# Kernel optimization log

Measured on AMD Instinct MI355X. Metric: run time of the kernel, lower is better.

Reference implementation:

```python
import jax, jax.numpy as jnp
import numpy as np
import math

N_HEADS = 12
ROPE_DIM = 64
BASE = 10000.0


def _rope_tables(seq_len, dim):
    inv_freq = 1.0 / (BASE ** (jnp.arange(0, dim, 2, dtype=jnp.float32) / dim))
    t = jnp.arange(seq_len, dtype=jnp.float32)
    freqs = jnp.outer(t, inv_freq)                      # [S, dim/2]
    emb = jnp.concatenate([freqs, freqs], axis=-1)      # [S, dim]
    # broadcast shape [1, S, 1, dim]
    return jnp.cos(emb)[None, :, None, :], jnp.sin(emb)[None, :, None, :]


def _rotate_half(x):
    x1, x2 = jnp.split(x, 2, axis=-1)
    return jnp.concatenate([-x2, x1], axis=-1)


def setup_inputs() -> dict:
    key = jax.random.key(0)
    ks = jax.random.split(key, 9)
    B, S, E = 2, 2048, 768
    s = 1.0 / math.sqrt(E)
    return {
        "x": jax.random.normal(ks[0], (B, S, E), jnp.float32),
        "Wq": jax.random.normal(ks[1], (E, E), jnp.float32) * s,
        "bq": jax.random.normal(ks[2], (E,), jnp.float32) * 0.02,
        "Wk": jax.random.normal(ks[3], (E, E), jnp.float32) * s,
        "bk": jax.random.normal(ks[4], (E,), jnp.float32) * 0.02,
        "Wv": jax.random.normal(ks[5], (E, E), jnp.float32) * s,
        "bv": jax.random.normal(ks[6], (E,), jnp.float32) * 0.02,
        "Wp": jax.random.normal(ks[7], (E, E), jnp.float32) * s,
        "bp": jax.random.normal(ks[8], (E,), jnp.float32) * 0.02,
    }


def reference(x, Wq, bq, Wk, bk, Wv, bv, Wp, bp):
    B, S, E = x.shape
    H = N_HEADS
    D = E // H

    q = (x @ Wq + bq).reshape(B, S, H, D)
    k = (x @ Wk + bk).reshape(B, S, H, D)
    v = (x @ Wv + bv).reshape(B, S, H, D)

    # rotary on first ROPE_DIM dims (here ROPE_DIM == D, so full rotary)
    cos, sin = _rope_tables(S, ROPE_DIM)
    q_rot, q_pass = q[..., :ROPE_DIM], q[..., ROPE_DIM:]
    k_rot, k_pass = k[..., :ROPE_DIM], k[..., ROPE_DIM:]
    q_rot = q_rot * cos + _rotate_half(q_rot) * sin
    k_rot = k_rot * cos + _rotate_half(k_rot) * sin
    q = jnp.concatenate([q_rot, q_pass], axis=-1)
    k = jnp.concatenate([k_rot, k_pass], axis=-1)

    # scores [B, M, N, H]; mask before scaling (as in the torch code; -inf unchanged)
    att = jnp.einsum("bmhd,bnhd->bmnh", q, k)
    causal = jnp.tril(jnp.ones((S, S), dtype=bool))[None, :, :, None]
    att = jnp.where(causal, att, -jnp.inf)
    att = jax.nn.softmax(att / math.sqrt(D), axis=2)
    out = jnp.einsum("bmnh,bnhd->bmhd", att, v)

    return out.reshape(B, S, E) @ Wp + bp
```

## Files before the change

kernel.cpp:

```cpp
#include <hip/hip_runtime.h>
#include <stdint.h>

#define S_LEN 2048
#define EMB   768
#define NH    12
#define DH    64
#define M_TOT 4096
#define WELEM 589824
#define QELEM 3145728

typedef float  floatx4 __attribute__((ext_vector_type(4)));
typedef __bf16 bf16x8  __attribute__((ext_vector_type(8)));
typedef __bf16 bf16x4  __attribute__((ext_vector_type(4)));
typedef unsigned short ushortx4 __attribute__((ext_vector_type(4)));

__device__ __forceinline__ unsigned short f2bf(float f) {
    union { float f; unsigned u; } v; v.f = f;
    unsigned u = v.u;
    unsigned r = (u + 0x7FFFu + ((u >> 16) & 1u)) >> 16;
    return (unsigned short)r;
}

__device__ __forceinline__ void gl_lds16(const void* g, void* l) {
    __builtin_amdgcn_global_load_lds(
        (__attribute__((address_space(1))) const void*)g,
        (__attribute__((address_space(3))) void*)l, 16, 0, 0);
}

__global__ void cvt_all_kernel(const float* __restrict__ x, unsigned short* __restrict__ xb,
                               const float* __restrict__ W0, const float* __restrict__ W1,
                               const float* __restrict__ W2, const float* __restrict__ W3,
                               unsigned short* __restrict__ WT_all) {
    __shared__ float t[64][65];
    const int blk = blockIdx.x;
    if (blk < 3072) {
        int i = (blk * 256 + threadIdx.x) * 4;
        float4 v = *(const float4*)(x + i);
        ushortx4 r = { f2bf(v.x), f2bf(v.y), f2bf(v.z), f2bf(v.w) };
        *(ushortx4*)(xb + i) = r;
        return;
    }
    const int tc = blk - 3072;
    const int z = tc / 144, rr0 = tc % 144;
    const float* W = (z == 0) ? W0 : (z == 1 ? W1 : (z == 2 ? W2 : W3));
    unsigned short* O = WT_all + (size_t)z * WELEM;
    const int k0 = (rr0 % 12) * 64, n0 = (rr0 / 12) * 64;
    const int c = threadIdx.x & 63, r4 = threadIdx.x >> 6;
#pragma unroll
    for (int rr = 0; rr < 64; rr += 4) {
        int r = rr + r4;
        t[r][c] = W[(size_t)(k0 + r) * EMB + n0 + c];
    }
    __syncthreads();
#pragma unroll
    for (int rr = 0; rr < 64; rr += 4) {
        int nn = rr + r4;
        O[(size_t)(n0 + nn) * EMB + k0 + c] = f2bf(t[c][nn]);
    }
}

static __device__ __forceinline__ void gemm_core_128x128(
    const unsigned short* __restrict__ A, const unsigned short* __restrict__ BT,
    int m0, int n0, int K, int tid, floatx4 (&acc)[4][4],
    unsigned short* Als, unsigned short* Bls)
{
    const int lane = tid & 63;
    const int c0 = lane & 15, quad = lane >> 4;
    const int wave = tid >> 6;
    const int wm = (wave >> 1) * 64, wn = (wave & 1) * 64;

    for (int k0 = 0; k0 < K; k0 += 64) {
        __syncthreads();
#pragma unroll
        for (int it = 0; it < 4; ++it) {
            int ch = it * 256 + tid;
            int row = ch >> 3, sc = ch & 7;
            int cc = sc ^ (row & 7);
            gl_lds16(A  + (size_t)(m0 + row) * K + k0 + cc * 8, Als + ch * 8);
            gl_lds16(BT + (size_t)(n0 + row) * K + k0 + cc * 8, Bls + ch * 8);
        }
        __syncthreads();
        bf16x8 af[4][2], bfv[4][2];
#pragma unroll
        for (int ii = 0; ii < 4; ++ii) {
            int row = wm + 16 * ii + c0;
#pragma unroll
            for (int h = 0; h < 2; ++h)
                af[ii][h] = *(const bf16x8*)(Als + row * 64 + (((4 * h + quad) ^ (row & 7)) * 8));
        }
#pragma unroll
        for (int jj = 0; jj < 4; ++jj) {
            int row = wn + 16 * jj + c0;
#pragma unroll
            for (int h = 0; h < 2; ++h)
                bfv[jj][h] = *(const bf16x8*)(Bls + row * 64 + (((4 * h + quad) ^ (row & 7)) * 8));
        }
#pragma unroll
        for (int ii = 0; ii < 4; ++ii)
#pragma unroll
            for (int jj = 0; jj < 4; ++jj) {
                acc[ii][jj] = __builtin_amdgcn_mfma_f32_16x16x32_bf16(af[ii][0], bfv[jj][0], acc[ii][jj], 0, 0, 0);
                acc[ii][jj] = __builtin_amdgcn_mfma_f32_16x16x32_bf16(af[ii][1], bfv[jj][1], acc[ii][jj], 0, 0, 0);
            }
    }
}

__global__ __launch_bounds__(256, 2) void qkv_kernel(
    const unsigned short* __restrict__ xb, const unsigned short* __restrict__ WT_all,
    const float* __restrict__ bq, const float* __restrict__ bk, const float* __restrict__ bv,
    unsigned short* __restrict__ qkv_out)
{
    __shared__ __align__(16) unsigned short Als[128 * 64];
    __shared__ __align__(16) unsigned short Bls[128 * 64];
    const int z = blockIdx.z;
    const float* bias = (z == 0) ? bq : (z == 1 ? bk : bv);
    __bf16* Cout = (__bf16*)(qkv_out + (size_t)z * QELEM);
    const int m0 = blockIdx.x * 128, n0 = blockIdx.y * 128;
    const int tid = threadIdx.x, lane = tid & 63, c0 = lane & 15, quad = lane >> 4, wave = tid >> 6;
    const int wm = (wave >> 1) * 64, wn = (wave & 1) * 64;

    floatx4 acc[4][4] = {};
    gemm_core_128x128(xb, WT_all + (size_t)z * WELEM, m0, n0, EMB, tid, acc, Als, Bls);

#pragma unroll
    for (int ii = 0; ii < 4; ++ii) {
#pragma unroll
        for (int r = 0; r < 4; ++r) {
            int m = m0 + wm + 16 * ii + quad * 4 + r;
            int b = m >> 11, s = m & (S_LEN - 1);
            float vals[4];
#pragma unroll
            for (int jj = 0; jj < 4; ++jj) vals[jj] = acc[ii][jj][r] + bias[n0 + wn + 16 * jj + c0];
            if (z < 2) {
#pragma unroll
                for (int jj = 0; jj < 2; ++jj) {
                    int d = 16 * jj + c0;
                    float f = exp2f((float)d * -0.41524101186092034f);
                    float th = (float)s * f;
                    float sn, cs; sincosf(th, &sn, &cs);
                    float lo = vals[jj], hi = vals[jj + 2];
                    vals[jj]     = lo * cs - hi * sn;
                    vals[jj + 2] = hi * cs + lo * sn;
                }
            }
            if (z == 0) {
#pragma unroll
                for (int jj = 0; jj < 4; ++jj) vals[jj] *= 0.18033688011112042f;
            }
#pragma unroll
            for (int jj = 0; jj < 4; ++jj) {
                int n = n0 + wn + 16 * jj + c0;
                int h = n >> 6, d = n & 63;
                if (z < 2)
                    Cout[((size_t)(b * NH + h) * S_LEN + s) * DH + d] = (__bf16)vals[jj];
                else
                    Cout[((size_t)(b * NH + h) * DH + d) * S_LEN + s] = (__bf16)vals[jj];
            }
        }
    }
}

__global__ __launch_bounds__(256, 2) void flash_kernel(
    const unsigned short* __restrict__ Qg, const unsigned short* __restrict__ Kg,
    const unsigned short* __restrict__ Vt, unsigned short* __restrict__ Og)
{
    __shared__ __align__(16) unsigned short Kls[2][64 * 64];
    __shared__ __align__(16) unsigned short Vls[2][64 * 64];
    __shared__ __align__(16) unsigned short Pls[4][16 * 72];

    const int i = blockIdx.x;
    const int kk = i >> 8, g = i & 255;
    const int r0 = (kk == 0) ? g : (kk == 1 ? 511 - g : 512 + g);
    const int qt = 31 - r0 / 24;
    const int bh = r0 % 24;
    const int b = bh / NH, h = bh % NH;
    const int m0 = qt * 64;
    const int tid = threadIdx.x, lane = tid & 63, wave = tid >> 6;
    const int c0 = lane & 15, quad = lane >> 4;
    const size_t base = (size_t)bh * S_LEN * DH;
    const int mrow = m0 + wave * 16 + c0;

    bf16x8 qf0 = *(const bf16x8*)(Qg + base + (size_t)mrow * DH + quad * 8);
    bf16x8 qf1 = *(const bf16x8*)(Qg + base + (size_t)mrow * DH + 32 + quad * 8);

    floatx4 oa[4] = {};
    float l_lane = 0.f;
    const float C = 23.083120654223414f;
    const int ntiles = qt + 1;

#pragma unroll
    for (int it = 0; it < 2; ++it) {
        int ch = it * 256 + tid;
        int row = ch >> 3, cc = (ch & 7) ^ (row & 7);
        gl_lds16(Kg + base + (size_t)row * DH + cc * 8, &Kls[0][ch * 8]);
        gl_lds16(Vt + base + (size_t)row * S_LEN + cc * 8, &Vls[0][ch * 8]);
    }

    for (int nt = 0; nt < ntiles; ++nt) {
        __syncthreads();
        if (nt + 1 < ntiles) {
            int n0 = (nt + 1) * 64, buf = (nt + 1) & 1;
#pragma unroll
            for (int it = 0; it < 2; ++it) {
                int ch = it * 256 + tid;
                int row = ch >> 3, cc = (ch & 7) ^ (row & 7);
                gl_lds16(Kg + base + (size_t)(n0 + row) * DH + cc * 8, &Kls[buf][ch * 8]);
                gl_lds16(Vt + base + (size_t)row * S_LEN + n0 + cc * 8, &Vls[buf][ch * 8]);
            }
        }
        const unsigned short* Kb = Kls[nt & 1];
        const unsigned short* Vb = Vls[nt & 1];

        floatx4 sa[4];
        const floatx4 zz = { 0.f, 0.f, 0.f, 0.f };
#pragma unroll
        for (int jj = 0; jj < 4; ++jj) {
            int row = 16 * jj + c0;
            bf16x8 k0 = *(const bf16x8*)(Kb + row * 64 + ((quad ^ (row & 7)) * 8));
            bf16x8 k1 = *(const bf16x8*)(Kb + row * 64 + (((4 + quad) ^ (row & 7)) * 8));
            sa[jj] = __builtin_amdgcn_mfma_f32_16x16x32_bf16(k0, qf0, zz, 0, 0, 0);
            sa[jj] = __builtin_amdgcn_mfma_f32_16x16x32_bf16(k1, qf1, sa[jj], 0, 0, 0);
        }
        if (nt == ntiles - 1) {
#pragma unroll
            for (int jj = 0; jj < 4; ++jj) {
                int nb = m0 + 16 * jj + quad * 4;
#pragma unroll
                for (int rr = 0; rr < 4; ++rr)
                    if (nb + rr > mrow) sa[jj][rr] = -1e30f;
            }
        }
#pragma unroll
        for (int jj = 0; jj < 4; ++jj) {
            bf16x4 pw;
#pragma unroll
            for (int rr = 0; rr < 4; ++rr) {
                float p = __builtin_amdgcn_exp2f(sa[jj][rr] - C);
                l_lane += p;
                pw[rr] = (__bf16)p;
            }
            *(bf16x4*)(&Pls[wave][c0 * 72 + 16 * jj + quad * 4]) = pw;
        }
#pragma unroll
        for (int h2 = 0; h2 < 2; ++h2) {
            bf16x8 pf = *(const bf16x8*)(&Pls[wave][c0 * 72 + 32 * h2 + quad * 8]);
#pragma unroll
            for (int dt = 0; dt < 4; ++dt) {
                int row = 16 * dt + c0;
                bf16x8 vf = *(const bf16x8*)(Vb + row * 64 + (((4 * h2 + quad) ^ (row & 7)) * 8));
                oa[dt] = __builtin_amdgcn_mfma_f32_16x16x32_bf16(vf, pf, oa[dt], 0, 0, 0);
            }
        }
    }

    l_lane += __shfl_xor(l_lane, 16, 64);
    l_lane += __shfl_xor(l_lane, 32, 64);
    const float rl = 1.0f / l_lane;
    __bf16* Ob16 = (__bf16*)Og;
#pragma unroll
    for (int dt = 0; dt < 4; ++dt) {
        bf16x4 ov;
#pragma unroll
        for (int rr = 0; rr < 4; ++rr) ov[rr] = (__bf16)(oa[dt][rr] * rl);
        *(bf16x4*)(Ob16 + ((size_t)(b * S_LEN + mrow)) * EMB + h * DH + dt * 16 + quad * 4) = ov;
    }
}

__global__ __launch_bounds__(256, 2) void proj_kernel(
    const unsigned short* __restrict__ Ob, const unsigned short* __restrict__ WpT,
    const float* __restrict__ bp, float* __restrict__ out)
{
    __shared__ __align__(16) unsigned short Als[128 * 64];
    __shared__ __align__(16) unsigned short Bls[128 * 64];
    const int m0 = blockIdx.x * 128, n0 = blockIdx.y * 128;
    const int tid = threadIdx.x, lane = tid & 63, c0 = lane & 15, quad = lane >> 4, wave = tid >> 6;
    const int wm = (wave >> 1) * 64, wn = (wave & 1) * 64;

    floatx4 acc[4][4] = {};
    gemm_core_128x128(Ob, WpT, m0, n0, EMB, tid, acc, Als, Bls);

#pragma unroll
    for (int ii = 0; ii < 4; ++ii)
#pragma unroll
        for (int r = 0; r < 4; ++r) {
            int m = m0 + wm + 16 * ii + quad * 4 + r;
#pragma unroll
            for (int jj = 0; jj < 4; ++jj) {
                int n = n0 + wn + 16 * jj + c0;
                out[(size_t)m * EMB + n] = acc[ii][jj][r] + bp[n];
            }
        }
}

extern "C" void kernel_launch(void* const* d_in, const int* in_sizes, int n_in,
                              void* d_out, int out_size, void* d_ws, size_t ws_size,
                              hipStream_t stream)
{
    (void)in_sizes; (void)n_in; (void)out_size;
    const float* x  = (const float*)d_in[0];
    const float* Wq = (const float*)d_in[1];
    const float* bq = (const float*)d_in[2];
    const float* Wk = (const float*)d_in[3];
    const float* bk = (const float*)d_in[4];
    const float* Wv = (const float*)d_in[5];
    const float* bv = (const float*)d_in[6];
    const float* Wp = (const float*)d_in[7];
    const float* bp = (const float*)d_in[8];

    unsigned short* ws  = (unsigned short*)d_ws;
    unsigned short* xb  = ws;
    unsigned short* WT  = xb + (size_t)QELEM;
    unsigned short* QKV = WT + 4 * (size_t)WELEM;
    unsigned short* Ob  = QKV + 3 * (size_t)QELEM;
    if (ws_size < ((size_t)QELEM * 5 + 4 * (size_t)WELEM) * 2) return;

    cvt_all_kernel<<<3648, 256, 0, stream>>>(x, xb, Wq, Wk, Wv, Wp, WT);
    qkv_kernel<<<dim3(32, 6, 3), 256, 0, stream>>>(xb, WT, bq, bk, bv, QKV);
    flash_kernel<<<dim3(768), 256, 0, stream>>>(QKV, QKV + QELEM, QKV + 2 * (size_t)QELEM, Ob);
    proj_kernel<<<dim3(32, 6), 256, 0, stream>>>(Ob, WT + 3 * (size_t)WELEM, bp, (float*)d_out);
}
```

Before: 155.9 us.

## Precompute RoPE table, vectorize V store, raise flash occupancy, add MFMA priority

The cvt kernel now also fills a cos/sin table for all positions and frequencies, so the QKV epilogue does a table lookup instead of computing sincos per element. The V epilogue gets its own path that writes four consecutive sequence positions as one bf16x4 store into the transposed layout. The flash kernel's launch bound moves from 2 to 3 blocks per SM, and s_setprio raises wave priority around the MFMA sections. This adds table memory traffic and an extra register-pressure limit on the flash kernel.

Result: no change. 155.6 us (-0.2%).

```diff
diff --git a/kernel.cpp b/kernel.cpp
--- a/kernel.cpp
+++ b/kernel.cpp
@@ -30,7 +30,7 @@
 __global__ void cvt_all_kernel(const float* __restrict__ x, unsigned short* __restrict__ xb,
                                const float* __restrict__ W0, const float* __restrict__ W1,
                                const float* __restrict__ W2, const float* __restrict__ W3,
-                               unsigned short* __restrict__ WT_all) {
+                               unsigned short* __restrict__ WT_all, float2* __restrict__ rope) {
     __shared__ float t[64][65];
     const int blk = blockIdx.x;
     if (blk < 3072) {
@@ -40,6 +40,15 @@
         *(ushortx4*)(xb + i) = r;
         return;
     }
+    if (blk >= 3648) {
+        int idx = (blk - 3648) * 256 + threadIdx.x;
+        int s = idx >> 5, d = idx & 31;
+        float f = exp2f((float)d * -0.41524101186092034f);
+        float th = (float)s * f;
+        float sn, cs; sincosf(th, &sn, &cs);
+        rope[idx] = make_float2(cs, sn);
+        return;
+    }
     const int tc = blk - 3072;
     const int z = tc / 144, rr0 = tc % 144;
     const float* W = (z == 0) ? W0 : (z == 1 ? W1 : (z == 2 ? W2 : W3));
@@ -108,7 +117,7 @@
 __global__ __launch_bounds__(256, 2) void qkv_kernel(
     const unsigned short* __restrict__ xb, const unsigned short* __restrict__ WT_all,
     const float* __restrict__ bq, const float* __restrict__ bk, const float* __restrict__ bv,
-    unsigned short* __restrict__ qkv_out)
+    const float2* __restrict__ rope, unsigned short* __restrict__ qkv_out)
 {
     __shared__ __align__(16) unsigned short Als[128 * 64];
     __shared__ __align__(16) unsigned short Bls[128 * 64];
@@ -122,6 +131,25 @@
     floatx4 acc[4][4] = {};
     gemm_core_128x128(xb, WT_all + (size_t)z * WELEM, m0, n0, EMB, tid, acc, Als, Bls);
 
+    if (z == 2) {
+#pragma unroll
+        for (int ii = 0; ii < 4; ++ii) {
+            int m = m0 + wm + 16 * ii + quad * 4;
+            int b = m >> 11, s = m & (S_LEN - 1);
+#pragma unroll
+            for (int jj = 0; jj < 4; ++jj) {
+                int n = n0 + wn + 16 * jj + c0;
+                int h = n >> 6, d = n & 63;
+                float bn = bias[n];
+                bf16x4 pv;
+#pragma unroll
+                for (int r = 0; r < 4; ++r) pv[r] = (__bf16)(acc[ii][jj][r] + bn);
+                *(bf16x4*)(Cout + ((size_t)(b * NH + h) * DH + d) * S_LEN + s) = pv;
+            }
+        }
+        return;
+    }
+
 #pragma unroll
     for (int ii = 0; ii < 4; ++ii) {
 #pragma unroll
@@ -131,17 +159,13 @@
             float vals[4];
 #pragma unroll
             for (int jj = 0; jj < 4; ++jj) vals[jj] = acc[ii][jj][r] + bias[n0 + wn + 16 * jj + c0];
-            if (z < 2) {
-#pragma unroll
-                for (int jj = 0; jj < 2; ++jj) {
-                    int d = 16 * jj + c0;
-                    float f = exp2f((float)d * -0.41524101186092034f);
-                    float th = (float)s * f;
-                    float sn, cs; sincosf(th, &sn, &cs);
-                    float lo = vals[jj], hi = vals[jj + 2];
-                    vals[jj]     = lo * cs - hi * sn;
-                    vals[jj + 2] = hi * cs + lo * sn;
-                }
+#pragma unroll
+            for (int jj = 0; jj < 2; ++jj) {
+                int d = 16 * jj + c0;
+                float2 t = rope[s * 32 + d];
+                float lo = vals[jj], hi = vals[jj + 2];
+                vals[jj]     = lo * t.x - hi * t.y;
+                vals[jj + 2] = hi * t.x + lo * t.y;
             }
             if (z == 0) {
 #pragma unroll
@@ -151,16 +175,13 @@
             for (int jj = 0; jj < 4; ++jj) {
                 int n = n0 + wn + 16 * jj + c0;
                 int h = n >> 6, d = n & 63;
-                if (z < 2)
-                    Cout[((size_t)(b * NH + h) * S_LEN + s) * DH + d] = (__bf16)vals[jj];
-                else
-                    Cout[((size_t)(b * NH + h) * DH + d) * S_LEN + s] = (__bf16)vals[jj];
-            }
-        }
-    }
-}
-
-__global__ __launch_bounds__(256, 2) void flash_kernel(
+                Cout[((size_t)(b * NH + h) * S_LEN + s) * DH + d] = (__bf16)vals[jj];
+            }
+        }
+    }
+}
+
+__global__ __launch_bounds__(256, 3) void flash_kernel(
     const unsigned short* __restrict__ Qg, const unsigned short* __restrict__ Kg,
     const unsigned short* __restrict__ Vt, unsigned short* __restrict__ Og)
 {
@@ -213,6 +234,7 @@
 
         floatx4 sa[4];
         const floatx4 zz = { 0.f, 0.f, 0.f, 0.f };
+        __builtin_amdgcn_s_setprio(1);
 #pragma unroll
         for (int jj = 0; jj < 4; ++jj) {
             int row = 16 * jj + c0;
@@ -221,6 +243,7 @@
             sa[jj] = __builtin_amdgcn_mfma_f32_16x16x32_bf16(k0, qf0, zz, 0, 0, 0);
             sa[jj] = __builtin_amdgcn_mfma_f32_16x16x32_bf16(k1, qf1, sa[jj], 0, 0, 0);
         }
+        __builtin_amdgcn_s_setprio(0);
         if (nt == ntiles - 1) {
 #pragma unroll
             for (int jj = 0; jj < 4; ++jj) {
@@ -241,6 +264,7 @@
             }
             *(bf16x4*)(&Pls[wave][c0 * 72 + 16 * jj + quad * 4]) = pw;
         }
+        __builtin_amdgcn_s_setprio(1);
 #pragma unroll
         for (int h2 = 0; h2 < 2; ++h2) {
             bf16x8 pf = *(const bf16x8*)(&Pls[wave][c0 * 72 + 32 * h2 + quad * 8]);
@@ -251,6 +275,7 @@
                 oa[dt] = __builtin_amdgcn_mfma_f32_16x16x32_bf16(vf, pf, oa[dt], 0, 0, 0);
             }
         }
+        __builtin_amdgcn_s_setprio(0);
     }
 
     l_lane += __shfl_xor(l_lane, 16, 64);
@@ -312,10 +337,11 @@
     unsigned short* WT  = xb + (size_t)QELEM;
     unsigned short* QKV = WT + 4 * (size_t)WELEM;
     unsigned short* Ob  = QKV + 3 * (size_t)QELEM;
-    if (ws_size < ((size_t)QELEM * 5 + 4 * (size_t)WELEM) * 2) return;
-
-    cvt_all_kernel<<<3648, 256, 0, stream>>>(x, xb, Wq, Wk, Wv, Wp, WT);
-    qkv_kernel<<<dim3(32, 6, 3), 256, 0, stream>>>(xb, WT, bq, bk, bv, QKV);
+    float2* rope = (float2*)(Ob + (size_t)QELEM);
+    if (ws_size < ((size_t)QELEM * 5 + 4 * (size_t)WELEM) * 2 + 2048 * 32 * 8) return;
+
+    cvt_all_kernel<<<3904, 256, 0, stream>>>(x, xb, Wq, Wk, Wv, Wp, WT, rope);
+    qkv_kernel<<<dim3(32, 6, 3), 256, 0, stream>>>(xb, WT, bq, bk, bv, (const float2*)rope, QKV);
     flash_kernel<<<dim3(768), 256, 0, stream>>>(QKV, QKV + QELEM, QKV + 2 * (size_t)QELEM, Ob);
     proj_kernel<<<dim3(32, 6), 256, 0, stream>>>(Ob, WT + 3 * (size_t)WELEM, bp, (float*)d_out);
 }
```
